# Optimization experiments

Measured on AMD Instinct MI355X. Metric: run time of the kernel, lower is better.

The kernel has to match this reference:

```python
import jax, jax.numpy as jnp
import numpy as np

N_VERTS = 163842  # icosphere level-7 mesh
C = 128
K = 7  # vertex + 6 one-ring neighbors
BN_EPS = 1e-5


def setup_inputs() -> dict:
    key = jax.random.key(0)
    ks = jax.random.split(key, 4)
    x = jax.random.normal(ks[0], (N_VERTS, C), dtype=jnp.float32)
    neigh_orders = jax.random.randint(ks[1], (N_VERTS * K,), 0, N_VERTS, dtype=jnp.int64)
    W1 = jax.random.normal(ks[2], (C, K * C), dtype=jnp.float32) * 0.02
    b1 = jnp.zeros((C,), dtype=jnp.float32)
    gamma1 = jnp.ones((C,), dtype=jnp.float32)
    beta1 = jnp.zeros((C,), dtype=jnp.float32)
    W2 = jax.random.normal(ks[3], (C, K * C), dtype=jnp.float32) * 0.02
    b2 = jnp.zeros((C,), dtype=jnp.float32)
    gamma2 = jnp.ones((C,), dtype=jnp.float32)
    beta2 = jnp.zeros((C,), dtype=jnp.float32)
    return {"x": x, "neigh_orders": neigh_orders, "W1": W1, "b1": b1,
            "gamma1": gamma1, "beta1": beta1, "W2": W2, "b2": b2,
            "gamma2": gamma2, "beta2": beta2}


def _onering_conv(x, neigh_orders, W, b):
    # gather [N*7, C] -> [N, 7*C], then linear
    feat = x[neigh_orders].reshape(x.shape[0], -1)
    return feat @ W.T + b


def _batchnorm(h, gamma, beta):
    # training-mode BatchNorm1d over the vertex (batch) dim, biased variance
    mean = jnp.mean(h, axis=0)
    var = jnp.var(h, axis=0)
    return (h - mean) * jax.lax.rsqrt(var + BN_EPS) * gamma + beta


def _leaky_relu(h):
    return jnp.where(h >= 0, h, 0.2 * h)


def reference(x, neigh_orders, W1, b1, gamma1, beta1, W2, b2, gamma2, beta2):
    h = _onering_conv(x, neigh_orders, W1, b1)
    h = _leaky_relu(_batchnorm(h, gamma1, beta1))
    h = _onering_conv(h, neigh_orders, W2, b2)
    h = _batchnorm(h, gamma2, beta2)
    return _leaky_relu(h + x)  # first_in_block=False -> plain residual
```

## Files before the change

### kernel.cpp

```cpp
#include <hip/hip_runtime.h>

#define NV 163842
#define NC 128
#define KN 7
#define NWELT (NC * KN * NC)
#define BN_EPS 1e-5f
#define NBLK 1281
#define RG 32
#define RROWS 41

typedef __attribute__((ext_vector_type(4))) float f32x4;
typedef __attribute__((ext_vector_type(8))) short bf16x8;
typedef __attribute__((ext_vector_type(8))) unsigned short u16x8;

static __device__ __forceinline__ unsigned short f2bf(float f) {
    union { float f; unsigned int u; } v; v.f = f;
    unsigned int r = v.u + 0x7fffu + ((v.u >> 16) & 1u);
    return (unsigned short)(r >> 16);
}
static __device__ __forceinline__ float bf2f(unsigned short s) {
    union { unsigned int u; float f; } v; v.u = ((unsigned int)s) << 16;
    return v.f;
}
static __device__ __forceinline__ void gload_lds16(const void* g, void* l) {
    __builtin_amdgcn_global_load_lds((const __attribute__((address_space(1))) void*)g,
                                     (__attribute__((address_space(3))) void*)l, 16, 0, 0);
}

__global__ void cvt_kernel(const float* __restrict__ x, const float* __restrict__ w1,
                           const float* __restrict__ w2, unsigned short* __restrict__ xbf,
                           unsigned short* __restrict__ w1bf, unsigned short* __restrict__ w2bf)
{
    const int total4 = (NV * NC + 2 * NWELT) / 4;
    for (int i = blockIdx.x * blockDim.x + threadIdx.x; i < total4; i += gridDim.x * blockDim.x) {
        int e = i * 4;
        const float* src; unsigned short* dst;
        if (e < NV * NC)              { src = x  + e;                  dst = xbf  + e; }
        else if (e < NV * NC + NWELT) { src = w1 + (e - NV * NC);      dst = w1bf + (e - NV * NC); }
        else                          { src = w2 + (e - NV * NC - NWELT); dst = w2bf + (e - NV * NC - NWELT); }
        float4 v = *(const float4*)src;
        ushort4 o;
        o.x = f2bf(v.x); o.y = f2bf(v.y); o.z = f2bf(v.z); o.w = f2bf(v.w);
        *(ushort4*)dst = o;
    }
}

__global__ __launch_bounds__(512, 4)
void conv_kernel(const unsigned short* __restrict__ xin,
                 const int* __restrict__ neigh,
                 const unsigned short* __restrict__ wbf,
                 unsigned short* __restrict__ hout,
                 float* __restrict__ psum, float* __restrict__ psq)
{
    __shared__ __align__(16) char smem[65536];

    const int t    = threadIdx.x;
    const int row0 = blockIdx.x * 128;
    const int w    = t >> 6;
    const int lane = t & 63;
    const int lrow = lane & 15;
    const int lgrp = lane >> 4;
    const int wr   = w >> 2;
    const int wc   = w & 3;

    const int sl   = lane & 7;
    const int r3   = lane >> 3;
    const int srcoff = ((sl ^ r3) << 4);

    const int rA0 = w * 16 + r3;
    const int rA1 = w * 16 + 8 + r3;
    const int g0  = (row0 + rA0 < NV) ? (row0 + rA0) : (NV - 1);
    const int g1  = (row0 + rA1 < NV) ? (row0 + rA1) : (NV - 1);

    int idx0[KN], idx1[KN];
    #pragma unroll
    for (int k = 0; k < KN; ++k) {
        idx0[k] = neigh[g0 * KN + k];
        idx1[k] = neigh[g1 * KN + k];
    }

    const char* xinb = (const char*)xin;
    const char* wbfb = (const char*)wbf;
    const char* bsrc0 = wbfb + (size_t)(w * 16 + r3) * 1792 + srcoff;
    const char* bsrc1 = wbfb + (size_t)(w * 16 + 8 + r3) * 1792 + srcoff;

    f32x4 acc[4][2];
    #pragma unroll
    for (int mf = 0; mf < 4; ++mf)
        #pragma unroll
        for (int nf = 0; nf < 2; ++nf)
            acc[mf][nf] = (f32x4){0.f, 0.f, 0.f, 0.f};

#define STAGE(c) do {                                                              \
        const int h_ = (c) & 1, k_ = (c) >> 1, bs_ = ((c) & 1) * 32768;            \
        char* lA = smem + bs_ + w * 2048;                                          \
        char* lB = smem + bs_ + 16384 + w * 2048;                                  \
        gload_lds16(xinb + (size_t)idx0[k_] * 256 + h_ * 128 + srcoff, lA);        \
        gload_lds16(xinb + (size_t)idx1[k_] * 256 + h_ * 128 + srcoff, lA + 1024); \
        gload_lds16(bsrc0 + k_ * 256 + h_ * 128, lB);                              \
        gload_lds16(bsrc1 + k_ * 256 + h_ * 128, lB + 1024);                       \
    } while (0)

    STAGE(0);
    asm volatile("s_waitcnt vmcnt(0)" ::: "memory");
    __builtin_amdgcn_s_barrier();
    __builtin_amdgcn_sched_barrier(0);

    #pragma unroll
    for (int c = 0; c < 14; ++c) {
        if (c < 13) STAGE(c + 1);

        const char* Ab = smem + (c & 1) * 32768;
        const char* Bb = Ab + 16384;
        #pragma unroll
        for (int ks = 0; ks < 2; ++ks) {
            const int koff = ks * 64 + lgrp * 16;
            bf16x8 a[4], b[2];
            #pragma unroll
            for (int mf = 0; mf < 4; ++mf) {
                const int arow = wr * 64 + mf * 16 + lrow;
                a[mf] = *(const bf16x8*)(Ab + ((arow * 128 + koff) ^ ((arow & 7) << 4)));
            }
            #pragma unroll
            for (int nf = 0; nf < 2; ++nf) {
                const int bcol = wc * 32 + nf * 16 + lrow;
                b[nf] = *(const bf16x8*)(Bb + ((bcol * 128 + koff) ^ ((bcol & 7) << 4)));
            }
            #pragma unroll
            for (int mf = 0; mf < 4; ++mf)
                #pragma unroll
                for (int nf = 0; nf < 2; ++nf)
                    acc[mf][nf] = __builtin_amdgcn_mfma_f32_16x16x32_bf16(a[mf], b[nf], acc[mf][nf], 0, 0, 0);
        }

        asm volatile("s_waitcnt vmcnt(0)" ::: "memory");
        __builtin_amdgcn_sched_barrier(0);
        __builtin_amdgcn_s_barrier();
        __builtin_amdgcn_sched_barrier(0);
    }
#undef STAGE

    float* redsum = (float*)smem;
    float* redsq  = (float*)(smem + 1024);

    #pragma unroll
    for (int nf = 0; nf < 2; ++nf) {
        const int col = wc * 32 + nf * 16 + lrow;
        float sum = 0.f, sq = 0.f;
        #pragma unroll
        for (int mf = 0; mf < 4; ++mf) {
            const int rbase = row0 + wr * 64 + mf * 16 + lgrp * 4;
            #pragma unroll
            for (int r = 0; r < 4; ++r) {
                float v = acc[mf][nf][r];
                const int grow = rbase + r;
                if (grow < NV) {
                    sum += v; sq += v * v;
                    hout[(size_t)grow * NC + col] = f2bf(v);
                }
            }
        }
        sum += __shfl_xor(sum, 16); sum += __shfl_xor(sum, 32);
        sq  += __shfl_xor(sq, 16);  sq  += __shfl_xor(sq, 32);
        if (lgrp == 0) { redsum[wr * 128 + col] = sum; redsq[wr * 128 + col] = sq; }
    }
    __syncthreads();
    if (t < 128) {
        psum[(size_t)blockIdx.x * 128 + t] = redsum[t] + redsum[128 + t];
        psq[(size_t)blockIdx.x * 128 + t]  = redsq[t]  + redsq[128 + t];
    }
}

__global__ void bn_reduce_kernel(const float* __restrict__ psum, const float* __restrict__ psq,
                                 float* __restrict__ psum2, float* __restrict__ psq2)
{
    const int c = threadIdx.x;
    const int g = blockIdx.x;
    const int b0 = g * RROWS;
    const int b1 = (b0 + RROWS < NBLK) ? b0 + RROWS : NBLK;
    float s = 0.f, q = 0.f;
    for (int b = b0; b < b1; ++b) {
        s += psum[b * 128 + c];
        q += psq[b * 128 + c];
    }
    psum2[g * 128 + c] = s;
    psq2[g * 128 + c]  = q;
}

__global__ void bn_finalize_kernel(const float* __restrict__ psum2, const float* __restrict__ psq2,
                                   const float* __restrict__ gamma, const float* __restrict__ beta,
                                   float* __restrict__ scale, float* __restrict__ shift)
{
    const int c = threadIdx.x;
    float s = 0.f, q = 0.f;
    #pragma unroll
    for (int g = 0; g < RG; ++g) { s += psum2[g * 128 + c]; q += psq2[g * 128 + c]; }
    const float inv  = 1.f / (float)NV;
    const float mean = s * inv;
    const float var  = q * inv - mean * mean;
    const float sc   = gamma[c] * rsqrtf(var + BN_EPS);
    scale[c] = sc;
    shift[c] = beta[c] - mean * sc;
}

__global__ void bn_apply_kernel(const unsigned short* __restrict__ h, const float* __restrict__ scale,
                                const float* __restrict__ shift, unsigned short* __restrict__ outbf)
{
    __shared__ float ssc[NC], ssh[NC];
    if (threadIdx.x < NC) { ssc[threadIdx.x] = scale[threadIdx.x]; ssh[threadIdx.x] = shift[threadIdx.x]; }
    __syncthreads();
    const int total8 = NV * NC / 8;
    for (int i = blockIdx.x * blockDim.x + threadIdx.x; i < total8; i += gridDim.x * blockDim.x) {
        const int e = i * 8;
        const int c0 = e & (NC - 1);
        u16x8 v = *(const u16x8*)(h + e);
        u16x8 o;
        #pragma unroll
        for (int j = 0; j < 8; ++j) {
            float a = bf2f(v[j]) * ssc[c0 + j] + ssh[c0 + j];
            a = a >= 0.f ? a : 0.2f * a;
            o[j] = f2bf(a);
        }
        *(u16x8*)(outbf + e) = o;
    }
}

__global__ void final_kernel(const unsigned short* __restrict__ h, const float* __restrict__ x,
                             const float* __restrict__ scale, const float* __restrict__ shift,
                             float* __restrict__ out)
{
    __shared__ float ssc[NC], ssh[NC];
    if (threadIdx.x < NC) { ssc[threadIdx.x] = scale[threadIdx.x]; ssh[threadIdx.x] = shift[threadIdx.x]; }
    __syncthreads();
    const int total8 = NV * NC / 8;
    for (int i = blockIdx.x * blockDim.x + threadIdx.x; i < total8; i += gridDim.x * blockDim.x) {
        const int e = i * 8;
        const int c0 = e & (NC - 1);
        u16x8 v = *(const u16x8*)(h + e);
        float4 x0 = *(const float4*)(x + e);
        float4 x1 = *(const float4*)(x + e + 4);
        float xv[8] = {x0.x, x0.y, x0.z, x0.w, x1.x, x1.y, x1.z, x1.w};
        float ov[8];
        #pragma unroll
        for (int j = 0; j < 8; ++j) {
            float a = bf2f(v[j]) * ssc[c0 + j] + ssh[c0 + j] + xv[j];
            ov[j] = a >= 0.f ? a : 0.2f * a;
        }
        float4 o0 = {ov[0], ov[1], ov[2], ov[3]};
        float4 o1 = {ov[4], ov[5], ov[6], ov[7]};
        *(float4*)(out + e)     = o0;
        *(float4*)(out + e + 4) = o1;
    }
}

extern "C" void kernel_launch(void* const* d_in, const int* in_sizes, int n_in,
                              void* d_out, int out_size, void* d_ws, size_t ws_size,
                              hipStream_t stream)
{
    const float* x      = (const float*)d_in[0];
    const int*   neigh  = (const int*)d_in[1];
    const float* W1     = (const float*)d_in[2];
    const float* gamma1 = (const float*)d_in[4];
    const float* beta1  = (const float*)d_in[5];
    const float* W2     = (const float*)d_in[6];
    const float* gamma2 = (const float*)d_in[8];
    const float* beta2  = (const float*)d_in[9];

    unsigned short* h1pre = (unsigned short*)d_out;
    unsigned short* h1bn  = (unsigned short*)d_out + (size_t)NV * NC;
    float* out = (float*)d_out;

    char* ws = (char*)d_ws;
    size_t off = 0;
    unsigned short* xbf  = (unsigned short*)(ws + off); off += (size_t)NV * NC * 2;
    unsigned short* w1bf = (unsigned short*)(ws + off); off += NWELT * 2;
    unsigned short* w2bf = (unsigned short*)(ws + off); off += NWELT * 2;
    float* psum  = (float*)(ws + off); off += (size_t)NBLK * 128 * 4;
    float* psq   = (float*)(ws + off); off += (size_t)NBLK * 128 * 4;
    float* psum2 = (float*)(ws + off); off += RG * 128 * 4;
    float* psq2  = (float*)(ws + off); off += RG * 128 * 4;
    float* scale1 = (float*)(ws + off); off += 512;
    float* shift1 = (float*)(ws + off); off += 512;
    float* scale2 = (float*)(ws + off); off += 512;
    float* shift2 = (float*)(ws + off); off += 512;
    unsigned short* h2pre = xbf;

    cvt_kernel<<<2048, 256, 0, stream>>>(x, W1, W2, xbf, w1bf, w2bf);
    conv_kernel<<<NBLK, 512, 0, stream>>>(xbf, neigh, w1bf, h1pre, psum, psq);
    bn_reduce_kernel<<<RG, 128, 0, stream>>>(psum, psq, psum2, psq2);
    bn_finalize_kernel<<<1, 128, 0, stream>>>(psum2, psq2, gamma1, beta1, scale1, shift1);
    bn_apply_kernel<<<2048, 256, 0, stream>>>(h1pre, scale1, shift1, h1bn);
    conv_kernel<<<NBLK, 512, 0, stream>>>(h1bn, neigh, w2bf, h2pre, psum, psq);
    bn_reduce_kernel<<<RG, 128, 0, stream>>>(psum, psq, psum2, psq2);
    bn_finalize_kernel<<<1, 128, 0, stream>>>(psum2, psq2, gamma2, beta2, scale2, shift2);
    final_kernel<<<2048, 256, 0, stream>>>(h2pre, x, scale2, shift2, out);
}
```

Baseline: 206.6 us.

## Load conv weights directly to registers, deepen A pipeline, read bf16 residual

The conv kernel no longer stages weight (B) tiles through shared memory. Each wave loads its weight fragments straight into registers, double-buffered one step ahead. The gathered activation (A) tiles now use a 4-slot LDS ring prefetched three steps ahead, with partial vmcnt waits and s_setprio around the MFMA block, to hide gather latency. The final kernel can read the residual from the bf16 copy of x when workspace allows, which lowers residual precision in exchange for halving that read traffic.

```diff
diff --git a/kernel.cpp b/kernel.cpp
--- a/kernel.cpp
+++ b/kernel.cpp
@@ -65,12 +65,11 @@
 
     const int sl   = lane & 7;
     const int r3   = lane >> 3;
-    const int srcoff = ((sl ^ r3) << 4);
+    const int srcoff = (sl ^ r3) << 4;
 
     const int rA0 = w * 16 + r3;
-    const int rA1 = w * 16 + 8 + r3;
-    const int g0  = (row0 + rA0 < NV) ? (row0 + rA0) : (NV - 1);
-    const int g1  = (row0 + rA1 < NV) ? (row0 + rA1) : (NV - 1);
+    const int g0  = (row0 + rA0     < NV) ? (row0 + rA0)     : (NV - 1);
+    const int g1  = (row0 + rA0 + 8 < NV) ? (row0 + rA0 + 8) : (NV - 1);
 
     int idx0[KN], idx1[KN];
     #pragma unroll
@@ -80,9 +79,8 @@
     }
 
     const char* xinb = (const char*)xin;
-    const char* wbfb = (const char*)wbf;
-    const char* bsrc0 = wbfb + (size_t)(w * 16 + r3) * 1792 + srcoff;
-    const char* bsrc1 = wbfb + (size_t)(w * 16 + 8 + r3) * 1792 + srcoff;
+    const unsigned short* bb0 = wbf + (size_t)(wc * 32 + lrow) * (KN * NC) + lgrp * 8;
+    const unsigned short* bb1 = bb0 + (size_t)16 * (KN * NC);
 
     f32x4 acc[4][2];
     #pragma unroll
@@ -91,54 +89,63 @@
         for (int nf = 0; nf < 2; ++nf)
             acc[mf][nf] = (f32x4){0.f, 0.f, 0.f, 0.f};
 
-#define STAGE(c) do {                                                              \
-        const int h_ = (c) & 1, k_ = (c) >> 1, bs_ = ((c) & 1) * 32768;            \
-        char* lA = smem + bs_ + w * 2048;                                          \
-        char* lB = smem + bs_ + 16384 + w * 2048;                                  \
-        gload_lds16(xinb + (size_t)idx0[k_] * 256 + h_ * 128 + srcoff, lA);        \
-        gload_lds16(xinb + (size_t)idx1[k_] * 256 + h_ * 128 + srcoff, lA + 1024); \
-        gload_lds16(bsrc0 + k_ * 256 + h_ * 128, lB);                              \
-        gload_lds16(bsrc1 + k_ * 256 + h_ * 128, lB + 1024);                       \
+    bf16x8 breg[2][2][2];
+
+#define STAGE_A(c) do {                                                                \
+        char* lA_ = smem + ((c) & 3) * 16384 + w * 2048;                               \
+        gload_lds16(xinb + (size_t)idx0[(c) >> 1] * 256 + ((c) & 1) * 128 + srcoff, lA_);        \
+        gload_lds16(xinb + (size_t)idx1[(c) >> 1] * 256 + ((c) & 1) * 128 + srcoff, lA_ + 1024); \
     } while (0)
-
-    STAGE(0);
-    asm volatile("s_waitcnt vmcnt(0)" ::: "memory");
+#define LOADB(c) do {                                                  \
+        breg[(c) & 1][0][0] = *(const bf16x8*)(bb0 + (c) * 64);        \
+        breg[(c) & 1][0][1] = *(const bf16x8*)(bb1 + (c) * 64);        \
+        breg[(c) & 1][1][0] = *(const bf16x8*)(bb0 + (c) * 64 + 32);   \
+        breg[(c) & 1][1][1] = *(const bf16x8*)(bb1 + (c) * 64 + 32);   \
+    } while (0)
+
+    STAGE_A(0); STAGE_A(1); STAGE_A(2); LOADB(0);
+    asm volatile("s_waitcnt vmcnt(8)" ::: "memory");
+    __builtin_amdgcn_sched_barrier(0);
     __builtin_amdgcn_s_barrier();
     __builtin_amdgcn_sched_barrier(0);
 
     #pragma unroll
     for (int c = 0; c < 14; ++c) {
-        if (c < 13) STAGE(c + 1);
-
-        const char* Ab = smem + (c & 1) * 32768;
-        const char* Bb = Ab + 16384;
+        if (c < 13) LOADB(c + 1);
+        if (c < 11) STAGE_A(c + 3);
+        __builtin_amdgcn_sched_barrier(0);
+
+        const char* Ab = smem + (c & 3) * 16384;
+        __builtin_amdgcn_s_setprio(1);
         #pragma unroll
         for (int ks = 0; ks < 2; ++ks) {
             const int koff = ks * 64 + lgrp * 16;
-            bf16x8 a[4], b[2];
+            bf16x8 a[4];
             #pragma unroll
             for (int mf = 0; mf < 4; ++mf) {
                 const int arow = wr * 64 + mf * 16 + lrow;
                 a[mf] = *(const bf16x8*)(Ab + ((arow * 128 + koff) ^ ((arow & 7) << 4)));
             }
             #pragma unroll
-            for (int nf = 0; nf < 2; ++nf) {
-                const int bcol = wc * 32 + nf * 16 + lrow;
-                b[nf] = *(const bf16x8*)(Bb + ((bcol * 128 + koff) ^ ((bcol & 7) << 4)));
+            for (int mf = 0; mf < 4; ++mf) {
+                acc[mf][0] = __builtin_amdgcn_mfma_f32_16x16x32_bf16(a[mf], breg[c & 1][ks][0], acc[mf][0], 0, 0, 0);
+                acc[mf][1] = __builtin_amdgcn_mfma_f32_16x16x32_bf16(a[mf], breg[c & 1][ks][1], acc[mf][1], 0, 0, 0);
             }
-            #pragma unroll
-            for (int mf = 0; mf < 4; ++mf)
-                #pragma unroll
-                for (int nf = 0; nf < 2; ++nf)
-                    acc[mf][nf] = __builtin_amdgcn_mfma_f32_16x16x32_bf16(a[mf], b[nf], acc[mf][nf], 0, 0, 0);
-        }
-
-        asm volatile("s_waitcnt vmcnt(0)" ::: "memory");
-        __builtin_amdgcn_sched_barrier(0);
-        __builtin_amdgcn_s_barrier();
-        __builtin_amdgcn_sched_barrier(0);
-    }
-#undef STAGE
+        }
+        __builtin_amdgcn_s_setprio(0);
+
+        if (c < 13) {
+            __builtin_amdgcn_sched_barrier(0);
+            if (c <= 10)      asm volatile("s_waitcnt vmcnt(12)" ::: "memory");
+            else if (c == 11) asm volatile("s_waitcnt vmcnt(10)" ::: "memory");
+            else              asm volatile("s_waitcnt vmcnt(8)"  ::: "memory");
+            __builtin_amdgcn_sched_barrier(0);
+            __builtin_amdgcn_s_barrier();
+            __builtin_amdgcn_sched_barrier(0);
+        }
+    }
+#undef STAGE_A
+#undef LOADB
 
     float* redsum = (float*)smem;
     float* redsq  = (float*)(smem + 1024);
@@ -226,6 +233,7 @@
 }
 
 __global__ void final_kernel(const unsigned short* __restrict__ h, const float* __restrict__ x,
+                             const unsigned short* __restrict__ xb, const int use_bf,
                              const float* __restrict__ scale, const float* __restrict__ shift,
                              float* __restrict__ out)
 {
@@ -237,9 +245,17 @@
         const int e = i * 8;
         const int c0 = e & (NC - 1);
         u16x8 v = *(const u16x8*)(h + e);
-        float4 x0 = *(const float4*)(x + e);
-        float4 x1 = *(const float4*)(x + e + 4);
-        float xv[8] = {x0.x, x0.y, x0.z, x0.w, x1.x, x1.y, x1.z, x1.w};
+        float xv[8];
+        if (use_bf) {
+            u16x8 xvb = *(const u16x8*)(xb + e);
+            #pragma unroll
+            for (int j = 0; j < 8; ++j) xv[j] = bf2f(xvb[j]);
+        } else {
+            float4 x0 = *(const float4*)(x + e);
+            float4 x1 = *(const float4*)(x + e + 4);
+            xv[0]=x0.x; xv[1]=x0.y; xv[2]=x0.z; xv[3]=x0.w;
+            xv[4]=x1.x; xv[5]=x1.y; xv[6]=x1.z; xv[7]=x1.w;
+        }
         float ov[8];
         #pragma unroll
         for (int j = 0; j < 8; ++j) {
@@ -283,7 +299,12 @@
     float* shift1 = (float*)(ws + off); off += 512;
     float* scale2 = (float*)(ws + off); off += 512;
     float* shift2 = (float*)(ws + off); off += 512;
-    unsigned short* h2pre = xbf;
+
+    const size_t h2_bytes = (size_t)NV * NC * 2;
+    unsigned short* h2pre;
+    int use_bf;
+    if (off + h2_bytes <= ws_size) { h2pre = (unsigned short*)(ws + off); use_bf = 1; }
+    else                           { h2pre = xbf;                        use_bf = 0; }
 
     cvt_kernel<<<2048, 256, 0, stream>>>(x, W1, W2, xbf, w1bf, w2bf);
     conv_kernel<<<NBLK, 512, 0, stream>>>(xbf, neigh, w1bf, h1pre, psum, psq);
@@ -293,5 +314,5 @@
     conv_kernel<<<NBLK, 512, 0, stream>>>(h1bn, neigh, w2bf, h2pre, psum, psq);
     bn_reduce_kernel<<<RG, 128, 0, stream>>>(psum, psq, psum2, psq2);
     bn_finalize_kernel<<<1, 128, 0, stream>>>(psum2, psq2, gamma2, beta2, scale2, shift2);
-    final_kernel<<<2048, 256, 0, stream>>>(h2pre, x, scale2, shift2, out);
-}
+    final_kernel<<<2048, 256, 0, stream>>>(h2pre, x, xbf, use_bf, scale2, shift2, out);
+}
```

New measurement: 284.7 us. 37.8% more time.

## Halve conv LDS stage to raise occupancy and read bf16 residual when workspace allows

Applied to the files above, without the earlier changes.

The conv kernel now stages 32-wide K slices (28 stages instead of 14), which halves shared memory to 32KB. Each thread gathers one row with a single index array, and launch bounds rise to allow 8 blocks per CU. The aim is more waves in flight to hide gather latency, at the cost of twice as many barriers and waitcnts. The final kernel can also read the residual from the bf16 copy of x when workspace space lets h2 live elsewhere, which cuts residual read bytes but adds bf16 rounding to the residual add.

```diff
diff --git a/kernel.cpp b/kernel.cpp
--- a/kernel.cpp
+++ b/kernel.cpp
@@ -45,14 +45,14 @@
     }
 }
 
-__global__ __launch_bounds__(512, 4)
+__global__ __launch_bounds__(512, 8)
 void conv_kernel(const unsigned short* __restrict__ xin,
                  const int* __restrict__ neigh,
                  const unsigned short* __restrict__ wbf,
                  unsigned short* __restrict__ hout,
                  float* __restrict__ psum, float* __restrict__ psq)
 {
-    __shared__ __align__(16) char smem[65536];
+    __shared__ __align__(16) char smem[32768];
 
     const int t    = threadIdx.x;
     const int row0 = blockIdx.x * 128;
@@ -63,26 +63,17 @@
     const int wr   = w >> 2;
     const int wc   = w & 3;
 
-    const int sl   = lane & 7;
-    const int r3   = lane >> 3;
-    const int srcoff = ((sl ^ r3) << 4);
-
-    const int rA0 = w * 16 + r3;
-    const int rA1 = w * 16 + 8 + r3;
-    const int g0  = (row0 + rA0 < NV) ? (row0 + rA0) : (NV - 1);
-    const int g1  = (row0 + rA1 < NV) ? (row0 + rA1) : (NV - 1);
-
-    int idx0[KN], idx1[KN];
-    #pragma unroll
-    for (int k = 0; k < KN; ++k) {
-        idx0[k] = neigh[g0 * KN + k];
-        idx1[k] = neigh[g1 * KN + k];
-    }
+    const int srow = t >> 2;
+    const int sl   = t & 3;
+    const int srcoff = ((sl ^ ((srow >> 1) & 3)) << 4);
+
+    const int g = (row0 + srow < NV) ? (row0 + srow) : (NV - 1);
+    int idx[KN];
+    #pragma unroll
+    for (int k = 0; k < KN; ++k) idx[k] = neigh[g * KN + k];
 
     const char* xinb = (const char*)xin;
-    const char* wbfb = (const char*)wbf;
-    const char* bsrc0 = wbfb + (size_t)(w * 16 + r3) * 1792 + srcoff;
-    const char* bsrc1 = wbfb + (size_t)(w * 16 + 8 + r3) * 1792 + srcoff;
+    const char* bsrc = (const char*)wbf + (size_t)srow * 1792 + srcoff;
 
     f32x4 acc[4][2];
     #pragma unroll
@@ -91,14 +82,12 @@
         for (int nf = 0; nf < 2; ++nf)
             acc[mf][nf] = (f32x4){0.f, 0.f, 0.f, 0.f};
 
-#define STAGE(c) do {                                                              \
-        const int h_ = (c) & 1, k_ = (c) >> 1, bs_ = ((c) & 1) * 32768;            \
-        char* lA = smem + bs_ + w * 2048;                                          \
-        char* lB = smem + bs_ + 16384 + w * 2048;                                  \
-        gload_lds16(xinb + (size_t)idx0[k_] * 256 + h_ * 128 + srcoff, lA);        \
-        gload_lds16(xinb + (size_t)idx1[k_] * 256 + h_ * 128 + srcoff, lA + 1024); \
-        gload_lds16(bsrc0 + k_ * 256 + h_ * 128, lB);                              \
-        gload_lds16(bsrc1 + k_ * 256 + h_ * 128, lB + 1024);                       \
+#define STAGE(c) do {                                                               \
+        const int k_ = (c) >> 2, q_ = (c) & 3, bs_ = ((c) & 1) * 16384;             \
+        gload_lds16(xinb + (size_t)idx[k_] * 256 + q_ * 64 + srcoff,                \
+                    smem + bs_ + w * 1024);                                         \
+        gload_lds16(bsrc + k_ * 256 + q_ * 64,                                      \
+                    smem + bs_ + 8192 + w * 1024);                                  \
     } while (0)
 
     STAGE(0);
@@ -107,36 +96,34 @@
     __builtin_amdgcn_sched_barrier(0);
 
     #pragma unroll
-    for (int c = 0; c < 14; ++c) {
-        if (c < 13) STAGE(c + 1);
-
-        const char* Ab = smem + (c & 1) * 32768;
-        const char* Bb = Ab + 16384;
-        #pragma unroll
-        for (int ks = 0; ks < 2; ++ks) {
-            const int koff = ks * 64 + lgrp * 16;
-            bf16x8 a[4], b[2];
-            #pragma unroll
-            for (int mf = 0; mf < 4; ++mf) {
-                const int arow = wr * 64 + mf * 16 + lrow;
-                a[mf] = *(const bf16x8*)(Ab + ((arow * 128 + koff) ^ ((arow & 7) << 4)));
-            }
-            #pragma unroll
-            for (int nf = 0; nf < 2; ++nf) {
-                const int bcol = wc * 32 + nf * 16 + lrow;
-                b[nf] = *(const bf16x8*)(Bb + ((bcol * 128 + koff) ^ ((bcol & 7) << 4)));
-            }
-            #pragma unroll
-            for (int mf = 0; mf < 4; ++mf)
-                #pragma unroll
-                for (int nf = 0; nf < 2; ++nf)
-                    acc[mf][nf] = __builtin_amdgcn_mfma_f32_16x16x32_bf16(a[mf], b[nf], acc[mf][nf], 0, 0, 0);
-        }
-
-        asm volatile("s_waitcnt vmcnt(0)" ::: "memory");
-        __builtin_amdgcn_sched_barrier(0);
-        __builtin_amdgcn_s_barrier();
-        __builtin_amdgcn_sched_barrier(0);
+    for (int c = 0; c < 28; ++c) {
+        if (c < 27) STAGE(c + 1);
+
+        const char* Ab = smem + (c & 1) * 16384;
+        const char* Bb = Ab + 8192;
+        bf16x8 a[4], b[2];
+        #pragma unroll
+        for (int mf = 0; mf < 4; ++mf) {
+            const int arow = wr * 64 + mf * 16 + lrow;
+            a[mf] = *(const bf16x8*)(Ab + arow * 64 + ((lgrp ^ ((arow >> 1) & 3)) << 4));
+        }
+        #pragma unroll
+        for (int nf = 0; nf < 2; ++nf) {
+            const int bcol = wc * 32 + nf * 16 + lrow;
+            b[nf] = *(const bf16x8*)(Bb + bcol * 64 + ((lgrp ^ ((bcol >> 1) & 3)) << 4));
+        }
+        #pragma unroll
+        for (int mf = 0; mf < 4; ++mf) {
+            acc[mf][0] = __builtin_amdgcn_mfma_f32_16x16x32_bf16(a[mf], b[0], acc[mf][0], 0, 0, 0);
+            acc[mf][1] = __builtin_amdgcn_mfma_f32_16x16x32_bf16(a[mf], b[1], acc[mf][1], 0, 0, 0);
+        }
+
+        if (c < 27) {
+            asm volatile("s_waitcnt vmcnt(0)" ::: "memory");
+            __builtin_amdgcn_sched_barrier(0);
+            __builtin_amdgcn_s_barrier();
+            __builtin_amdgcn_sched_barrier(0);
+        }
     }
 #undef STAGE
 
@@ -226,6 +213,7 @@
 }
 
 __global__ void final_kernel(const unsigned short* __restrict__ h, const float* __restrict__ x,
+                             const unsigned short* __restrict__ xb, const int use_bf,
                              const float* __restrict__ scale, const float* __restrict__ shift,
                              float* __restrict__ out)
 {
@@ -237,9 +225,17 @@
         const int e = i * 8;
         const int c0 = e & (NC - 1);
         u16x8 v = *(const u16x8*)(h + e);
-        float4 x0 = *(const float4*)(x + e);
-        float4 x1 = *(const float4*)(x + e + 4);
-        float xv[8] = {x0.x, x0.y, x0.z, x0.w, x1.x, x1.y, x1.z, x1.w};
+        float xv[8];
+        if (use_bf) {
+            u16x8 xvb = *(const u16x8*)(xb + e);
+            #pragma unroll
+            for (int j = 0; j < 8; ++j) xv[j] = bf2f(xvb[j]);
+        } else {
+            float4 x0 = *(const float4*)(x + e);
+            float4 x1 = *(const float4*)(x + e + 4);
+            xv[0]=x0.x; xv[1]=x0.y; xv[2]=x0.z; xv[3]=x0.w;
+            xv[4]=x1.x; xv[5]=x1.y; xv[6]=x1.z; xv[7]=x1.w;
+        }
         float ov[8];
         #pragma unroll
         for (int j = 0; j < 8; ++j) {
@@ -283,7 +279,12 @@
     float* shift1 = (float*)(ws + off); off += 512;
     float* scale2 = (float*)(ws + off); off += 512;
     float* shift2 = (float*)(ws + off); off += 512;
-    unsigned short* h2pre = xbf;
+
+    const size_t h2_bytes = (size_t)NV * NC * 2;
+    unsigned short* h2pre;
+    int use_bf;
+    if (off + h2_bytes <= ws_size) { h2pre = (unsigned short*)(ws + off); use_bf = 1; }
+    else                           { h2pre = xbf;                        use_bf = 0; }
 
     cvt_kernel<<<2048, 256, 0, stream>>>(x, W1, W2, xbf, w1bf, w2bf);
     conv_kernel<<<NBLK, 512, 0, stream>>>(xbf, neigh, w1bf, h1pre, psum, psq);
@@ -293,5 +294,5 @@
     conv_kernel<<<NBLK, 512, 0, stream>>>(h1bn, neigh, w2bf, h2pre, psum, psq);
     bn_reduce_kernel<<<RG, 128, 0, stream>>>(psum, psq, psum2, psq2);
     bn_finalize_kernel<<<1, 128, 0, stream>>>(psum2, psq2, gamma2, beta2, scale2, shift2);
-    final_kernel<<<2048, 256, 0, stream>>>(h2pre, x, scale2, shift2, out);
-}
+    final_kernel<<<2048, 256, 0, stream>>>(h2pre, x, xbf, use_bf, scale2, shift2, out);
+}
```

New measurement: 263.0 us. +27.3%, slower.
